# Optimization experiments

Measured on AMD Instinct MI355X. Metric: run time of the kernel, lower is better.

## Reference

```python
import jax, jax.numpy as jnp
import numpy as np

T, B, N, G, M = 2, 16, 1024, 64, 32
D_MODEL, N_LAYER = 384, 12
D_INNER, D_STATE, DT_RANK, D_CONV = 768, 16, 24, 4
TAU, V_TH, SG_ALPHA, BN_EPS, LN_EPS = 2.0, 0.5, 4.0, 1e-5, 1e-5

@jax.custom_vjp
def heaviside(x):
    return (x >= 0.0).astype(x.dtype)

def _hv_fwd(x):
    return heaviside(x), x

def _hv_bwd(x, g):
    s = jax.nn.sigmoid(SG_ALPHA * x)
    return (g * SG_ALPHA * s * (1.0 - s),)

heaviside.defvjp(_hv_fwd, _hv_bwd)

def lif(x):
    # multi-step LIF over leading T folded into batch: x is [T*B, ...]
    shp = x.shape
    xt = x.reshape((T, shp[0] // T) + shp[1:])
    def step(v, xi):
        v = v + (xi - v) / TAU              # charge
        s = heaviside(v - V_TH)             # fire (surrogate grad)
        v = v * (1.0 - jax.lax.stop_gradient(s))  # detached hard reset
        return v, s
    _, spikes = jax.lax.scan(step, jnp.zeros_like(xt[0]), xt)
    return spikes.reshape(shp)

def bn(x, g, b):
    # eval-mode BatchNorm with running stats (mean 0, var 1)
    return x * (g / jnp.sqrt(1.0 + BN_EPS)) + b

def layernorm(x, g, b):
    mu = jnp.mean(x, -1, keepdims=True)
    var = jnp.var(x, -1, keepdims=True)
    return (x - mu) / jnp.sqrt(var + LN_EPS) * g + b

def fps(pts, n_samples):
    # pts: [B, N, 3]; serial farthest point sampling starting at index 0
    b = pts.shape[0]
    def step(carry, _):
        dist, last = carry
        lp = jnp.take_along_axis(pts, last[:, None, None], axis=1)
        d = jnp.sum((pts - lp) ** 2, -1)
        dist = jnp.minimum(dist, d)
        nxt = jnp.argmax(dist, -1).astype(jnp.int32)
        return (dist, nxt), last
    init = (jnp.full((b, pts.shape[1]), 1e10, pts.dtype), jnp.zeros((b,), jnp.int32))
    _, idxs = jax.lax.scan(step, init, None, length=n_samples)
    return jnp.take_along_axis(pts, idxs.T[..., None], axis=1)

def mamba(x, in_w, conv_w, conv_b, xproj_w, dt_w, dt_b, A_log, Dp, out_w):
    # x: [TB, L, d_model] spiking-Mamba mixer
    tb, L, _ = x.shape
    xz = x @ in_w.T
    xh, z = jnp.split(xz, 2, axis=-1)                     # [TB, L, Di]
    xc = jnp.transpose(xh, (0, 2, 1))                     # [TB, Di, L]
    xc = jax.lax.conv_general_dilated(xc, conv_w[:, None, :], (1,), [(D_CONV - 1, 0)], dimension_numbers=('NCH', 'OIH', 'NCH'), feature_group_count=D_INNER) + conv_b[None, :, None]
    xs = lif(jnp.transpose(xc, (0, 2, 1)))                # spiking activation
    dbl = xs @ xproj_w.T
    dt, Bm, Cm = jnp.split(dbl, [DT_RANK, DT_RANK + D_STATE], axis=-1)
    dt = jax.nn.softplus(dt @ dt_w.T + dt_b)              # [TB, L, Di]
    A = -jnp.exp(A_log)                                   # [Di, S]
    def step(h, inp):
        dt_t, B_t, C_t, x_t = inp
        h = h * jnp.exp(dt_t[..., None] * A) + (dt_t * x_t)[..., None] * B_t[:, None, :]
        y = jnp.einsum('bds,bs->bd', h, C_t)
        return h, y
    h0 = jnp.zeros((tb, D_INNER, D_STATE), x.dtype)
    _, ys = jax.lax.scan(step, h0, (dt.transpose(1, 0, 2), Bm.transpose(1, 0, 2), Cm.transpose(1, 0, 2), xs.transpose(1, 0, 2)))
    y = ys.transpose(1, 0, 2) + xs * Dp                   # [TB, L, Di]
    y = y * lif(z)                                        # spiking gate
    return y @ out_w.T

def _forward(xyz, enc1_w, enc1_b, bn1_g, bn1_b, enc2_w, enc2_b, bn2_g, bn2_b, enc3_w, enc3_b, bn3_g, bn3_b, enc4_w, enc4_b, bn4_g, bn4_b, pos1_w, pos1_b, pos2_w, pos2_b, in_w, conv_w, conv_b, xproj_w, dt_w, dt_b, A_log, Dp, out_w, normf_g, normf_b):
    xyz_f = xyz.reshape(T * B, N, 3)
    # Group: FPS centers (expand=1.0 -> identical centers per timestep) + KNN gather
    center = jnp.tile(fps(xyz_f[:B], G), (T, 1, 1))       # [TB, G, 3]
    d2 = jnp.sum(center ** 2, -1)[..., None] + jnp.sum(xyz_f ** 2, -1)[:, None, :] - 2.0 * jnp.einsum('bgc,bnc->bgn', center, xyz_f)
    _, idx = jax.lax.top_k(-d2, M)                        # [TB, G, M]
    nb = jax.vmap(lambda p, i: p[i])(xyz_f, idx)          # [TB, G, M, 3]
    nb = nb - center[:, :, None, :]
    # Encoder (1x1 convs == matmuls over last dim), BN eval-mode, LIF spikes
    f = bn(nb @ enc1_w.T + enc1_b, bn1_g, bn1_b)
    f = lif(f)
    f = bn(f @ enc2_w.T + enc2_b, bn2_g, bn2_b)           # [TB, G, M, 256]
    gl = jnp.max(f, axis=2, keepdims=True)
    f = jnp.concatenate([jnp.broadcast_to(gl, f.shape), f], axis=-1)  # 512 ch
    f = lif(f)
    f = bn(f @ enc3_w.T + enc3_b, bn3_g, bn3_b)
    f = lif(f)
    f = bn(f @ enc4_w.T + enc4_b, bn4_g, bn4_b)
    tokens = jnp.max(f, axis=2)                           # [TB, G, d_model]
    pos = jax.nn.gelu(center @ pos1_w.T + pos1_b) @ pos2_w.T + pos2_b
    hidden = tokens + pos
    residual = None
    for l in range(N_LAYER):
        residual = hidden if residual is None else hidden + residual
        hs = lif(residual)                                # Block.norm_lif
        hidden = mamba(hs, in_w[l], conv_w[l], conv_b[l], xproj_w[l], dt_w[l], dt_b[l], A_log[l], Dp[l], out_w[l])
    residual = hidden + residual
    return layernorm(residual, normf_g, normf_b)          # [TB, G, d_model]

def setup_inputs():
    key = jax.random.key(0)
    ks = iter(jax.random.split(key, 40))
    def nrm(shape, std):
        return jax.random.normal(next(ks), shape, jnp.float32) * std
    inp = {}
    inp['xyz'] = jax.random.normal(next(ks), (T, B, N, 3), jnp.float32)
    inp['enc1_w'] = nrm((128, 3), 0.5); inp['enc1_b'] = jnp.zeros((128,))
    inp['bn1_g'] = jnp.ones((128,)); inp['bn1_b'] = jnp.zeros((128,))
    inp['enc2_w'] = nrm((256, 128), 128 ** -0.5); inp['enc2_b'] = jnp.zeros((256,))
    inp['bn2_g'] = jnp.ones((256,)); inp['bn2_b'] = jnp.zeros((256,))
    inp['enc3_w'] = nrm((512, 512), 512 ** -0.5); inp['enc3_b'] = jnp.zeros((512,))
    inp['bn3_g'] = jnp.ones((512,)); inp['bn3_b'] = jnp.zeros((512,))
    inp['enc4_w'] = nrm((D_MODEL, 512), 512 ** -0.5); inp['enc4_b'] = jnp.zeros((D_MODEL,))
    inp['bn4_g'] = jnp.ones((D_MODEL,)); inp['bn4_b'] = jnp.zeros((D_MODEL,))
    inp['pos1_w'] = nrm((128, 3), 0.5); inp['pos1_b'] = jnp.zeros((128,))
    inp['pos2_w'] = nrm((D_MODEL, 128), 128 ** -0.5); inp['pos2_b'] = jnp.zeros((D_MODEL,))
    nl = N_LAYER
    inp['in_w'] = nrm((nl, 2 * D_INNER, D_MODEL), D_MODEL ** -0.5)
    inp['conv_w'] = nrm((nl, D_INNER, D_CONV), D_CONV ** -0.5)
    inp['conv_b'] = jnp.zeros((nl, D_INNER))
    inp['xproj_w'] = nrm((nl, DT_RANK + 2 * D_STATE, D_INNER), D_INNER ** -0.5)
    inp['dt_w'] = nrm((nl, D_INNER, DT_RANK), DT_RANK ** -0.5)
    inp['dt_b'] = jnp.full((nl, D_INNER), float(np.log(np.expm1(0.01))))
    inp['A_log'] = jnp.log(jnp.tile(jnp.arange(1, D_STATE + 1, dtype=jnp.float32), (nl, D_INNER, 1)))
    inp['Dp'] = jnp.ones((nl, D_INNER))
    inp['out_w'] = nrm((nl, D_MODEL, D_INNER), D_INNER ** -0.5)
    inp['normf_g'] = jnp.ones((D_MODEL,)); inp['normf_b'] = jnp.zeros((D_MODEL,))
    return inp

def reference(xyz, enc1_w, enc1_b, bn1_g, bn1_b, enc2_w, enc2_b, bn2_g, bn2_b, enc3_w, enc3_b, bn3_g, bn3_b, enc4_w, enc4_b, bn4_g, bn4_b, pos1_w, pos1_b, pos2_w, pos2_b, in_w, conv_w, conv_b, xproj_w, dt_w, dt_b, A_log, Dp, out_w, normf_g, normf_b):
    return _forward(xyz, enc1_w, enc1_b, bn1_g, bn1_b, enc2_w, enc2_b, bn2_g, bn2_b, enc3_w, enc3_b, bn3_g, bn3_b, enc4_w, enc4_b, bn4_g, bn4_b, pos1_w, pos1_b, pos2_w, pos2_b, in_w, conv_w, conv_b, xproj_w, dt_w, dt_b, A_log, Dp, out_w, normf_g, normf_b)
```

## Files before the change

### kernel.cpp

```cpp
#include <hip/hip_runtime.h>
#include <hip/hip_bf16.h>

typedef unsigned short ushort_t;
typedef short short8 __attribute__((ext_vector_type(8)));
typedef float f32x4 __attribute__((ext_vector_type(4)));

#define T_    2
#define B_    16
#define NPTS  1024
#define G_    64
#define M_    32
#define DM    384
#define NLAYER 12
#define DI    768
#define DS    16
#define DTR   24
#define DCONV 4
#define TB    32
#define KSPL  6
#define OKC   4
#define LOG2E 1.4426950408889634f

#if __has_builtin(__builtin_amdgcn_exp2f)
#define EXP2F(x) __builtin_amdgcn_exp2f(x)
#else
#define EXP2F(x) exp2f(x)
#endif

__device__ __forceinline__ ushort_t f2b(float x) {
    unsigned u = __float_as_uint(x);
    u = (u + 0x7FFF + ((u >> 16) & 1)) >> 16;
    return (ushort_t)u;
}
__device__ __forceinline__ float b2f(ushort_t h) { return __uint_as_float(((unsigned)h) << 16); }
#define BF1 0x3F80

#define LIF2(va0, vb0, va1, vb1, O0, O1) do { \
    float _u = (va0)*0.5f; float _s = (_u >= 0.5f) ? 1.f : 0.f; _u = (_s > 0.f) ? 0.f : _u; \
    float _u2 = _u + ((vb0) - _u)*0.5f; \
    unsigned _r0 = (_s > 0.f) ? (unsigned)BF1 : 0u; \
    unsigned _r1 = (_u2 >= 0.5f) ? (unsigned)BF1 : 0u; \
    _u = (va1)*0.5f; _s = (_u >= 0.5f) ? 1.f : 0.f; _u = (_s > 0.f) ? 0.f : _u; \
    _u2 = _u + ((vb1) - _u)*0.5f; \
    O0 = _r0 | (((_s > 0.f) ? (unsigned)BF1 : 0u) << 16); \
    O1 = _r1 | (((_u2 >= 0.5f) ? (unsigned)BF1 : 0u) << 16); \
} while (0)

#define DPP_AMAX(bv, bi, CTRL) { \
    float _ov = __int_as_float(__builtin_amdgcn_update_dpp(__float_as_int(bv), __float_as_int(bv), CTRL, 0xF, 0xF, false)); \
    int   _oi = __builtin_amdgcn_update_dpp(bi, bi, CTRL, 0xF, 0xF, false); \
    bool _tk = (_ov > bv) || (_ov == bv && _oi < bi); \
    bv = _tk ? _ov : bv; bi = _tk ? _oi : bi; }
#define DPP_AMIN(bv, bi, CTRL) { \
    float _ov = __int_as_float(__builtin_amdgcn_update_dpp(__float_as_int(bv), __float_as_int(bv), CTRL, 0xF, 0xF, false)); \
    int   _oi = __builtin_amdgcn_update_dpp(bi, bi, CTRL, 0xF, 0xF, false); \
    bool _tk = (_ov < bv) || (_ov == bv && _oi < bi); \
    bv = _tk ? _ov : bv; bi = _tk ? _oi : bi; }
#define DPP_FADD(p, CTRL) { \
    float _ov = __int_as_float(__builtin_amdgcn_update_dpp(__float_as_int(p), __float_as_int(p), CTRL, 0xF, 0xF, false)); \
    p += _ov; }

__global__ __launch_bounds__(64) void fps_kernel(const float* __restrict__ xyz,
                                                 float* __restrict__ centers) {
    int b = blockIdx.x;
    const float* pts = xyz + (size_t)b * NPTS * 3;
    __shared__ float sx[NPTS], sy[NPTS], sz[NPTS];
    int t = threadIdx.x;
    for (int i = t; i < NPTS; i += 64) {
        sx[i] = pts[i*3+0]; sy[i] = pts[i*3+1]; sz[i] = pts[i*3+2];
    }
    __syncthreads();
    float px[16], py[16], pz[16], dd[16];
#pragma unroll
    for (int j = 0; j < 16; j++) {
        px[j] = sx[j*64+t]; py[j] = sy[j*64+t]; pz[j] = sz[j*64+t];
        dd[j] = 1e10f;
    }
    float lx = sx[0], ly = sy[0], lz = sz[0];
    for (int s = 0; s < G_; s++) {
        if (t == 0) {
            centers[(b*G_+s)*3+0] = lx;
            centers[(b*G_+s)*3+1] = ly;
            centers[(b*G_+s)*3+2] = lz;
        }
        float v[16]; int id[16];
#pragma unroll
        for (int j = 0; j < 16; j++) {
            float dx = px[j]-lx, dy = py[j]-ly, dz = pz[j]-lz;
            float di2 = dx*dx + dy*dy + dz*dz;
            dd[j] = fminf(dd[j], di2);
            v[j] = dd[j]; id[j] = j*64 + t;
        }
#pragma unroll
        for (int st = 8; st; st >>= 1)
#pragma unroll
            for (int j = 0; j < 8; j++) {
                if (j < st && v[j+st] > v[j]) { v[j] = v[j+st]; id[j] = id[j+st]; }
            }
        float bv = v[0]; int bi = id[0];
        DPP_AMAX(bv, bi, 0xB1);
        DPP_AMAX(bv, bi, 0x4E);
        DPP_AMAX(bv, bi, 0x141);
        DPP_AMAX(bv, bi, 0x140);
        {
            float ov = __shfl_xor(bv, 16); int oi = __shfl_xor(bi, 16);
            bool tk = (ov > bv) || (ov == bv && oi < bi);
            bv = tk ? ov : bv; bi = tk ? oi : bi;
            ov = __shfl_xor(bv, 32); oi = __shfl_xor(bi, 32);
            tk = (ov > bv) || (ov == bv && oi < bi);
            bv = tk ? ov : bv; bi = tk ? oi : bi;
        }
        lx = sx[bi]; ly = sy[bi]; lz = sz[bi];
    }
}

__global__ __launch_bounds__(256) void knn_kernel(const float* __restrict__ xyz,
                                                  const float* __restrict__ centers,
                                                  float* __restrict__ nb) {
    int tb = blockIdx.x >> 4;
    int g  = ((blockIdx.x & 15) << 2) + (threadIdx.x >> 6);
    const float* pts = xyz + (size_t)tb * NPTS * 3;
    int bb = tb & (B_-1);
    float cx = centers[(bb*G_+g)*3+0], cy = centers[(bb*G_+g)*3+1], cz = centers[(bb*G_+g)*3+2];
    float cs = cx*cx + cy*cy + cz*cz;
    __shared__ float sx[NPTS], sy[NPTS], sz[NPTS];
    int t = threadIdx.x & 63;
    for (int i = threadIdx.x; i < NPTS; i += 256) {
        sx[i] = pts[i*3+0]; sy[i] = pts[i*3+1]; sz[i] = pts[i*3+2];
    }
    __syncthreads();
    float d2[16];
#pragma unroll
    for (int j = 0; j < 16; j++) {
        int i = j*64 + t;
        float qx = sx[i], qy = sy[i], qz = sz[i];
        float ps  = qx*qx + qy*qy + qz*qz;
        float dot = cx*qx + cy*qy + cz*qz;
        d2[j] = cs + ps - 2.0f*dot;
    }
    for (int m = 0; m < M_; m++) {
        float v[16]; int id[16];
#pragma unroll
        for (int j = 0; j < 16; j++) { v[j] = d2[j]; id[j] = j*64 + t; }
#pragma unroll
        for (int st = 8; st; st >>= 1)
#pragma unroll
            for (int j = 0; j < 8; j++) {
                if (j < st && v[j+st] < v[j]) { v[j] = v[j+st]; id[j] = id[j+st]; }
            }
        float bv = v[0]; int bi = id[0];
        DPP_AMIN(bv, bi, 0xB1);
        DPP_AMIN(bv, bi, 0x4E);
        DPP_AMIN(bv, bi, 0x141);
        DPP_AMIN(bv, bi, 0x140);
        {
            float ov = __shfl_xor(bv, 16); int oi = __shfl_xor(bi, 16);
            bool tk = (ov < bv) || (ov == bv && oi < bi);
            bv = tk ? ov : bv; bi = tk ? oi : bi;
            ov = __shfl_xor(bv, 32); oi = __shfl_xor(bi, 32);
            tk = (ov < bv) || (ov == bv && oi < bi);
            bv = tk ? ov : bv; bi = tk ? oi : bi;
        }
        if ((bi & 63) == t) {
            int jw = bi >> 6;
#pragma unroll
            for (int j = 0; j < 16; j++) if (j == jw) d2[j] = 1e38f;
        }
        if (t == 0) {
            size_t o = (((size_t)tb * G_ + g) * M_ + m) * 3;
            nb[o+0] = sx[bi] - cx;
            nb[o+1] = sy[bi] - cy;
            nb[o+2] = sz[bi] - cz;
        }
    }
}

__global__ void wsplit3_kernel(const float* __restrict__ s0, int n0,
                               const float* __restrict__ s1, int n1,
                               const float* __restrict__ s2, int n2,
                               ushort_t* __restrict__ hi, ushort_t* __restrict__ lo) {
    int n = n0 + n1 + n2;
    for (int i = blockIdx.x*256 + threadIdx.x; i < n; i += gridDim.x*256) {
        float w = (i < n0) ? s0[i] : (i < n0+n1 ? s1[i-n0] : s2[i-n0-n1]);
        ushort_t h = f2b(w);
        hi[i] = h;
        lo[i] = f2b(w - b2f(h));
    }
}

template<int PRODS, int EPI, int BMR, int NB = 128>
__global__ __launch_bounds__(256) void gemm_mfma(
    const ushort_t* __restrict__ A, const ushort_t* __restrict__ Al, int lda,
    const ushort_t* __restrict__ Bh, const ushort_t* __restrict__ Bl, int ldb,
    const float* __restrict__ bias, const float* __restrict__ bng, const float* __restrict__ bnb,
    const float* __restrict__ extra, int extra_shift,
    float* __restrict__ out, int ldo,
    ushort_t* __restrict__ sout, int ldso, int half,
    int rows, int K, int Cout)
{
    constexpr int WN = (BMR == 128) ? 2 : 4;
    constexpr int BANDN = NB / WN;
    constexpr int JF = BANDN / 16;
    constexpr int SMSZ = BMR*64 + NB*64*2 + ((PRODS == 3) ? BMR*64 : 8);
    __shared__ __align__(16) ushort_t SMEM[SMSZ];
    ushort_t* As  = SMEM;
    ushort_t* Bhs = SMEM + BMR*64;
    ushort_t* Bls = Bhs + NB*64;
    ushort_t* Als = Bls + NB*64;
    const int tid = threadIdx.x;
    const int bx = blockIdx.x;
    const int by = blockIdx.y;
    int cb = by, kc = 0;
    if constexpr (EPI == 8) {
        int nbc = Cout / NB;
        cb = by % nbc; kc = by / nbc;
    }
    const int c0 = (EPI == 7) ? 0 : cb * NB;
    const int r0  = bx * BMR;
    const int r0h = bx * (BMR/2);
    const int lane = tid & 63, w = tid >> 6;
    const int wm = w / WN, wn = w % WN;
    const int lrow = lane & 15, lkg = lane >> 4;
    const int sw = (lrow & 7) << 3;

    f32x4 acc[4][JF];
#pragma unroll
    for (int i = 0; i < 4; i++)
#pragma unroll
        for (int j = 0; j < JF; j++) acc[i][j] = (f32x4){0.f, 0.f, 0.f, 0.f};

    const int kchu = (EPI == 8) ? (K / extra_shift) : 0;
    const int kbeg = (EPI == 7) ? by * half : ((EPI == 8) ? kc * kchu : 0);
    const int kend = (EPI == 7) ? kbeg + half : ((EPI == 8) ? kbeg + kchu : K);
    for (int k0 = kbeg; k0 < kend; k0 += 64) {
        __syncthreads();
        for (int s = tid; s < BMR*8; s += 256) {
            int row = s >> 3, kq = s & 7;
            int li = row*64 + ((kq*8) ^ ((row & 7) << 3));
            int grow;
            if constexpr (EPI == 0 || EPI == 6 || EPI == 7) grow = r0 + row;
            else {
                int q = row >> 4, wr = row & 15;
                grow = r0h + q*8 + (wr & 7) + ((wr & 8) ? half : 0);
            }
            *(uint4*)&As[li] = *(const uint4*)(A + (size_t)grow*lda + k0 + kq*8);
            if constexpr (PRODS == 3)
                *(uint4*)&Als[li] = *(const uint4*)(Al + (size_t)grow*lda + k0 + kq*8);
        }
        for (int s = tid; s < NB*8; s += 256) {
            int row = s >> 3, kq = s & 7;
            int li = row*64 + ((kq*8) ^ ((row & 7) << 3));
            uint4 vh = make_uint4(0,0,0,0), vl = make_uint4(0,0,0,0);
            if (c0 + row < Cout) {
                vh = *(const uint4*)(Bh + (size_t)(c0+row)*ldb + k0 + kq*8);
                vl = *(const uint4*)(Bl + (size_t)(c0+row)*ldb + k0 + kq*8);
            }
            *(uint4*)&Bhs[li] = vh;
            *(uint4*)&Bls[li] = vl;
        }
        __syncthreads();
#pragma unroll
        for (int kc2 = 0; kc2 < 2; kc2++) {
            const int kb = (kc2*32 + lkg*8) ^ sw;
            short8 af[4], bhf[JF], blf[JF];
#pragma unroll
            for (int tI = 0; tI < 4; tI++)
                af[tI]  = *(const short8*)&As [(wm*64 + tI*16 + lrow)*64 + kb];
#pragma unroll
            for (int tJ = 0; tJ < JF; tJ++) {
                bhf[tJ] = *(const short8*)&Bhs[(wn*BANDN + tJ*16 + lrow)*64 + kb];
                blf[tJ] = *(const short8*)&Bls[(wn*BANDN + tJ*16 + lrow)*64 + kb];
            }
#pragma unroll
            for (int i = 0; i < 4; i++)
#pragma unroll
                for (int j = 0; j < JF; j++)
                    acc[i][j] = __builtin_amdgcn_mfma_f32_16x16x32_bf16(af[i], bhf[j], acc[i][j], 0, 0, 0);
#pragma unroll
            for (int i = 0; i < 4; i++)
#pragma unroll
                for (int j = 0; j < JF; j++)
                    acc[i][j] = __builtin_amdgcn_mfma_f32_16x16x32_bf16(af[i], blf[j], acc[i][j], 0, 0, 0);
            if constexpr (PRODS == 3) {
                short8 alf[4];
#pragma unroll
                for (int tI = 0; tI < 4; tI++)
                    alf[tI] = *(const short8*)&Als[(wm*64 + tI*16 + lrow)*64 + kb];
#pragma unroll
                for (int i = 0; i < 4; i++)
#pragma unroll
                    for (int j = 0; j < JF; j++)
                        acc[i][j] = __builtin_amdgcn_mfma_f32_16x16x32_bf16(alf[i], bhf[j], acc[i][j], 0, 0, 0);
            }
        }
    }

    const float rbn = 1.0f / sqrtf(1.0f + 1e-5f);
    const int ocol0 = c0 + wn*BANDN + lrow;
    auto spike_pair = [&](float vt) -> ushort_t {
        float vp = __shfl_xor(vt, 32);
        float x0 = (lane < 32) ? vt : vp;
        float x1 = (lane < 32) ? vp : vt;
        float u  = x0 * 0.5f;
        float s0 = (u >= 0.5f) ? 1.f : 0.f;
        u = (s0 > 0.f) ? 0.f : u;
        float u2 = u + (x1 - u) * 0.5f;
        return (lane < 32) ? ((s0 > 0.f) ? BF1 : 0) : ((u2 >= 0.5f) ? BF1 : 0);
    };

    if constexpr (EPI == 0) {
#pragma unroll
        for (int j = 0; j < JF; j++) {
            int col = ocol0 + j*16;
            if (col >= Cout) continue;
            float bsc = 1.f, bsh = 0.f, bv = 0.f;
            if (bng)  { bsc = bng[col] * rbn; bsh = bnb[col]; }
            if (bias) bv = bias[col];
#pragma unroll
            for (int i = 0; i < 4; i++)
#pragma unroll
                for (int r = 0; r < 4; r++) {
                    int grow = r0 + wm*64 + i*16 + lkg*4 + r;
                    float v = acc[i][j][r];
                    if (extra) v += extra[(size_t)(grow >> extra_shift)*Cout + col];
                    v += bv;
                    if (bng) v = v*bsc + bsh;
                    out[(size_t)grow*ldo + col] = v;
                }
        }
    }

    if constexpr (EPI == 7) {
        float* op = out + (size_t)by * rows * ldo;
#pragma unroll
        for (int j = 0; j < JF; j++) {
            int col = ocol0 + j*16;
            if (col >= Cout) continue;
#pragma unroll
            for (int i = 0; i < 4; i++)
#pragma unroll
                for (int r = 0; r < 4; r++) {
                    int grow = r0 + wm*64 + i*16 + lkg*4 + r;
                    op[(size_t)grow*ldo + col] = acc[i][j][r];
                }
        }
    }

    if constexpr (EPI == 8) {
        float* op = out + (size_t)kc * rows * ldo;
#pragma unroll
        for (int j = 0; j < JF; j++) {
            int col = ocol0 + j*16;
#pragma unroll
            for (int i = 0; i < 4; i++)
#pragma unroll
                for (int r = 0; r < 4; r++) {
                    int orow_t = wm*64 + i*16 + lkg*4 + r;
                    int q = orow_t >> 4, wr = orow_t & 15;
                    int grow = r0h + q*8 + (wr & 7) + ((wr & 8) ? half : 0);
                    op[(size_t)grow*ldo + col] = acc[i][j][r];
                }
        }
    }

    if constexpr (EPI == 6) {
#pragma unroll
        for (int j = 0; j < JF; j++) {
            int col = ocol0 + j*16;
            float bsc = bng[col] * rbn, bsh = bnb[col], bv = bias[col];
            float m0 = -3.0e38f, m1 = -3.0e38f;
#pragma unroll
            for (int i = 0; i < 4; i++)
#pragma unroll
                for (int r = 0; r < 4; r++) {
                    float v = (acc[i][j][r] + bv) * bsc + bsh;
                    if (i < 2) m0 = fmaxf(m0, v); else m1 = fmaxf(m1, v);
                }
            m0 = fmaxf(m0, __shfl_xor(m0, 16)); m0 = fmaxf(m0, __shfl_xor(m0, 32));
            m1 = fmaxf(m1, __shfl_xor(m1, 16)); m1 = fmaxf(m1, __shfl_xor(m1, 32));
            int bg = (r0 >> 5) + wm*2;
            int msk = (1 << half) - 1;
            if (lkg == 0)
                out[(size_t)(bg >> half)*(G_*DM) + (size_t)(bg & msk)*ldo + col] = m0;
            else if (lkg == 1)
                out[(size_t)((bg+1) >> half)*(G_*DM) + (size_t)((bg+1) & msk)*ldo + col] = m1;
        }
    }

    if constexpr (EPI == 5) {
#pragma unroll
        for (int j = 0; j < JF; j++) {
            int col = ocol0 + j*16;
            float bsc = bng[col] * rbn, bsh = bnb[col], bv = bias[col];
            float gm = -3.0e38f;
#pragma unroll
            for (int i = 0; i < 4; i++)
#pragma unroll
                for (int r = 0; r < 4; r++) {
                    float v = (acc[i][j][r] + bv) * bsc + bsh;
                    gm = fmaxf(gm, v);
                }
            float g2 = fmaxf(gm, __shfl_xor(gm, 16));
            ushort_t gsp = spike_pair(g2);
            ushort_t* gout = (ushort_t*)out;
            int bg = (r0h >> 5) + wm;
            int prs = half >> 5;
            if (lane < 16) gout[(size_t)bg * 256 + col] = gsp;
            else if (lane >= 32 && lane < 48) gout[(size_t)(prs + bg) * 256 + col] = gsp;
        }
    }

    if constexpr (EPI == 2 || EPI == 5) {
        if constexpr (NB == 128) {
            __syncthreads();
            float* Ef = (float*)Bhs;
#pragma unroll
            for (int p = 0; p < 2; p++) {
                if (wn == p) {
#pragma unroll
                    for (int j = 0; j < JF; j++) {
                        int col = ocol0 + j*16;
                        float bsc = 1.f, bsh = 0.f, bv = 0.f;
                        if (bng) { bsc = bng[col] * rbn; bsh = bnb[col]; }
                        if (bias) bv = bias[col];
#pragma unroll
                        for (int i = 0; i < 4; i++)
#pragma unroll
                            for (int r = 0; r < 4; r++) {
                                int o = wm*64 + i*16 + lkg*4 + r;
                                int pr = ((o >> 4) << 3) + (o & 7);
                                int tt = (o >> 3) & 1;
                                float v = acc[i][j][r];
                                if (EPI == 2 && extra) {
                                    int grw = r0h + pr + (tt ? half : 0);
                                    v += extra[(size_t)(grw >> extra_shift)*Cout + col];
                                }
                                v += bv;
                                if (bng) v = v*bsc + bsh;
                                int lr = tt*64 + pr;
                                int cc = j*16 + lrow;
                                Ef[lr*64 + (cc ^ (((lr >> 2) & 3) << 4))] = v;
                            }
                    }
                }
                __syncthreads();
                {
                    int pr2 = tid >> 2, cs = tid & 3;
                    int sw2 = ((pr2 >> 2) & 3) << 4;
                    const float* E0 = Ef + pr2*64;
                    const float* E1 = Ef + (64 + pr2)*64;
                    int colg = c0 + p*64 + cs*16;
                    ushort_t* s0p = sout + (size_t)(r0h + pr2)*ldso + colg;
                    ushort_t* s1p = s0p + (size_t)half*ldso;
#pragma unroll
                    for (int h = 0; h < 4; h++) {
                        int cb2 = (cs*16 + h*4) ^ sw2;
                        const float* e0 = E0 + cb2;
                        const float* e1 = E1 + cb2;
                        unsigned oa, ob, pa, pb;
                        LIF2(e0[0], e1[0], e0[1], e1[1], oa, pa);
                        LIF2(e0[2], e1[2], e0[3], e1[3], ob, pb);
                        *(uint2*)(s0p + h*4) = make_uint2(oa, ob);
                        *(uint2*)(s1p + h*4) = make_uint2(pa, pb);
                    }
                }
                if (p == 0) __syncthreads();
            }
        } else {
            __syncthreads();
            float* Ef = (float*)As;
#pragma unroll
            for (int j = 0; j < JF; j++) {
                int col = ocol0 + j*16;
                float bsc = 1.f, bsh = 0.f, bv = 0.f;
                if (bng) { bsc = bng[col] * rbn; bsh = bnb[col]; }
                if (bias) bv = bias[col];
#pragma unroll
                for (int i = 0; i < 4; i++)
#pragma unroll
                    for (int r = 0; r < 4; r++) {
                        int o = wm*64 + i*16 + lkg*4 + r;
                        int pr = ((o >> 4) << 3) + (o & 7);
                        int tt = (o >> 3) & 1;
                        float v = acc[i][j][r];
                        if (EPI == 2 && extra) {
                            int grw = r0h + pr + (tt ? half : 0);
                            v += extra[(size_t)(grw >> extra_shift)*Cout + col];
                        }
                        v += bv;
                        if (bng) v = v*bsc + bsh;
                        int lr = tt*64 + pr;
                        int cc = wn*BANDN + j*16 + lrow;
                        Ef[lr*64 + (cc ^ (((lr >> 2) & 3) << 4))] = v;
                    }
            }
            __syncthreads();
            {
                int pr2 = tid >> 2, cs = tid & 3;
                int sw2 = ((pr2 >> 2) & 3) << 4;
                const float* E0 = Ef + pr2*64;
                const float* E1 = Ef + (64 + pr2)*64;
                int colg = c0 + cs*16;
                ushort_t* s0p = sout + (size_t)(r0h + pr2)*ldso + colg;
                ushort_t* s1p = s0p + (size_t)half*ldso;
#pragma unroll
                for (int h = 0; h < 4; h++) {
                    int cb2 = (cs*16 + h*4) ^ sw2;
                    const float* e0 = E0 + cb2;
                    const float* e1 = E1 + cb2;
                    unsigned oa, ob, pa, pb;
                    LIF2(e0[0], e1[0], e0[1], e1[1], oa, pa);
                    LIF2(e0[2], e1[2], e0[3], e1[3], ob, pb);
                    *(uint2*)(s0p + h*4) = make_uint2(oa, ob);
                    *(uint2*)(s1p + h*4) = make_uint2(pa, pb);
                }
            }
        }
    }

    if constexpr (EPI == 4) {
        __syncthreads();
        float* Ef = (float*)Bhs;
#pragma unroll
        for (int j = 0; j < JF; j++) {
#pragma unroll
            for (int i = 0; i < 4; i++)
#pragma unroll
                for (int r = 0; r < 4; r++) {
                    int o = i*16 + lkg*4 + r;
                    int pr = ((o >> 4) << 3) + (o & 7);
                    int tt = (o >> 3) & 1;
                    int lr = tt*32 + pr;
                    int cc = wn*BANDN + j*16 + lrow;
                    Ef[lr*NB + (cc ^ (((lr >> 2) & 3) << 4))] = acc[i][j][r];
                }
        }
        __syncthreads();
        {
            constexpr int HH = NB / 32;
            constexpr int CPT = NB / 8;
            int pr2 = tid >> 3, cs = tid & 7;
            int sw2 = ((pr2 >> 2) & 3) << 4;
            const float* E0 = Ef + pr2*NB;
            const float* E1 = Ef + (32 + pr2)*NB;
            float* o0p = out + (size_t)(r0h + pr2)*ldo + c0 + cs*CPT;
            float* o1p = out + (size_t)(half + r0h + pr2)*ldo + c0 + cs*CPT;
            ushort_t* s0p = sout + (size_t)(r0h + pr2)*ldso + c0 + cs*CPT;
            ushort_t* s1p = sout + (size_t)(half + r0h + pr2)*ldso + c0 + cs*CPT;
#pragma unroll
            for (int h = 0; h < HH; h++) {
                int cb2 = (cs*CPT + h*4) ^ sw2;
                const float* e0 = E0 + cb2;
                const float* e1 = E1 + cb2;
                float4 rv0 = *(float4*)(o0p + h*4);
                float4 rv1 = *(float4*)(o1p + h*4);
                float t0x = e0[0]+rv0.x, t0y = e0[1]+rv0.y, t0z = e0[2]+rv0.z, t0w = e0[3]+rv0.w;
                float t1x = e1[0]+rv1.x, t1y = e1[1]+rv1.y, t1z = e1[2]+rv1.z, t1w = e1[3]+rv1.w;
                *(float4*)(o0p + h*4) = make_float4(t0x, t0y, t0z, t0w);
                *(float4*)(o1p + h*4) = make_float4(t1x, t1y, t1z, t1w);
                unsigned oa, ob, pa, pb;
                LIF2(t0x, t1x, t0y, t1y, oa, pa);
                LIF2(t0z, t1z, t0w, t1w, ob, pb);
                *(uint2*)(s0p + h*4) = make_uint2(oa, ob);
                *(uint2*)(s1p + h*4) = make_uint2(pa, pb);
            }
        }
    }

    if constexpr (EPI == 3) {
        if (c0 >= DI) {
#pragma unroll
            for (int j = 0; j < JF; j++) {
                int col = ocol0 + j*16;
#pragma unroll
                for (int i = 0; i < 4; i++)
#pragma unroll
                    for (int r = 0; r < 4; r++) {
                        int orow_t = wm*64 + i*16 + lkg*4 + r;
                        int q = orow_t >> 4, wr = orow_t & 15;
                        int grow = r0h + q*8 + (wr & 7) + ((wr & 8) ? half : 0);
                        sout[(size_t)grow*ldso + col - DI] = spike_pair(acc[i][j][r]);
                    }
            }
        } else {
            __syncthreads();
            constexpr int GRP = 256 / NB;
            constexpr int LPT = 64 / GRP;
            constexpr int SWM = (NB == 128) ? 7 : 3;
            float* Sme = wm ? (float*)Bls : (float*)Bhs;
            ushort_t* Asu = As;
            if (lkg < 2) {
#pragma unroll
                for (int j = 0; j < JF; j++) {
                    int dloc = wn*BANDN + j*16 + lrow;
#pragma unroll
                    for (int i = 0; i < 4; i++) {
                        int lr0 = i*8 + lkg*4;
#pragma unroll
                        for (int r = 0; r < 4; r++)
                            Sme[(lr0 + r)*NB + dloc] = acc[i][j][r];
                    }
                }
            }
            __syncthreads();
            const int dloc_c = tid & (NB - 1);
            const int lb = (tid / NB) * LPT;
            const int dg = c0 + dloc_c;
            const float cw0 = extra[dg*4+0], cw1 = extra[dg*4+1];
            const float cw2 = extra[dg*4+2], cw3 = extra[dg*4+3];
            const float cbv = bias[dg];
            const float* S0f = (const float*)Bhs;
            const float* S1f = (const float*)Bls;
            auto SRD = [&](int l) -> float {
                return (l < 32) ? S0f[l*NB + dloc_c] : S1f[(l - 32)*NB + dloc_c];
            };
            float a0[LPT];
            {
                float vm3 = 0.f, vm2 = 0.f, vm1 = 0.f;
                if (lb) { vm3 = SRD(lb-3); vm2 = SRD(lb-2); vm1 = SRD(lb-1); }
#pragma unroll
                for (int q = 0; q < LPT; q++) {
                    float v = SRD(lb + q);
                    float aa = vm3*cw0 + vm2*cw1 + vm1*cw2 + v*cw3 + cbv;
                    vm3 = vm2; vm2 = vm1; vm1 = v;
                    float u = aa * 0.5f;
                    float sv = (u >= 0.5f) ? 1.f : 0.f;
                    a0[q] = (sv > 0.f) ? 0.f : u;
                    int l = lb + q;
                    Asu[l*NB + (dloc_c ^ (((l >> 1) & SWM) << 4))] = (sv > 0.f) ? BF1 : 0;
                }
            }
            __syncthreads();
            if (lkg >= 2) {
#pragma unroll
                for (int j = 0; j < JF; j++) {
                    int dloc = wn*BANDN + j*16 + lrow;
#pragma unroll
                    for (int i = 0; i < 4; i++) {
                        int lr0 = i*8 + (lkg - 2)*4;
#pragma unroll
                        for (int r = 0; r < 4; r++)
                            Sme[(lr0 + r)*NB + dloc] = acc[i][j][r];
                    }
                }
            }
            ushort_t* xb0 = (ushort_t*)out + (size_t)bx * G_ * DI + c0;
            constexpr int CPT = NB / 4;
            {
                int row = tid >> 2, cs2 = tid & 3;
                int sw2 = ((row >> 1) & SWM) << 4;
                ushort_t* xrow = xb0 + (size_t)row * DI;
#pragma unroll
                for (int kk = 0; kk < NB/64; kk++) {
                    int cb2 = cs2*CPT + kk*16;
                    int cl = cb2 ^ sw2;
                    uint4 va = *(uint4*)&Asu[row*NB + cl];
                    uint4 vb = *(uint4*)&Asu[row*NB + cl + 8];
                    *(uint4*)&xrow[cb2] = va;
                    *(uint4*)&xrow[cb2 + 8] = vb;
                }
            }
            __syncthreads();
            {
                float vm3 = 0.f, vm2 = 0.f, vm1 = 0.f;
                if (lb) { vm3 = SRD(lb-3); vm2 = SRD(lb-2); vm1 = SRD(lb-1); }
#pragma unroll
                for (int q = 0; q < LPT; q++) {
                    float v = SRD(lb + q);
                    float a1 = vm3*cw0 + vm2*cw1 + vm1*cw2 + v*cw3 + cbv;
                    vm3 = vm2; vm2 = vm1; vm1 = v;
                    float u2 = a0[q] + (a1 - a0[q]) * 0.5f;
                    int l = lb + q;
                    Asu[l*NB + (dloc_c ^ (((l >> 1) & SWM) << 4))] = (u2 >= 0.5f) ? BF1 : 0;
                }
            }
            __syncthreads();
            {
                int row = tid >> 2, cs2 = tid & 3;
                int sw2 = ((row >> 1) & SWM) << 4;
                ushort_t* xrow = xb0 + (size_t)16 * G_ * DI + (size_t)row * DI;
#pragma unroll
                for (int kk = 0; kk < NB/64; kk++) {
                    int cb2 = cs2*CPT + kk*16;
                    int cl = cb2 ^ sw2;
                    uint4 va = *(uint4*)&Asu[row*NB + cl];
                    uint4 vb = *(uint4*)&Asu[row*NB + cl + 8];
                    *(uint4*)&xrow[cb2] = va;
                    *(uint4*)&xrow[cb2 + 8] = vb;
                }
            }
        }
    }
}

__global__ __launch_bounds__(256) void opfix_kernel(
    const float* __restrict__ part,
    float* __restrict__ residual, ushort_t* __restrict__ hs) {
    int e = blockIdx.x * 256 + threadIdx.x;
    if (e >= 1024 * (DM/4)) return;
    int r = e / (DM/4), c4 = (e % (DM/4)) * 4;
    size_t o0 = (size_t)r * DM + c4;
    size_t o1 = (size_t)(r + 1024) * DM + c4;
    float4 s0 = *(const float4*)(part + o0);
    float4 s1 = *(const float4*)(part + o1);
#pragma unroll
    for (int k = 1; k < OKC; k++) {
        float4 p0 = *(const float4*)(part + (size_t)k*2048*DM + o0);
        float4 p1 = *(const float4*)(part + (size_t)k*2048*DM + o1);
        s0.x += p0.x; s0.y += p0.y; s0.z += p0.z; s0.w += p0.w;
        s1.x += p1.x; s1.y += p1.y; s1.z += p1.z; s1.w += p1.w;
    }
    float4 rv0 = *(float4*)(residual + o0);
    float4 rv1 = *(float4*)(residual + o1);
    float t0x = s0.x+rv0.x, t0y = s0.y+rv0.y, t0z = s0.z+rv0.z, t0w = s0.w+rv0.w;
    float t1x = s1.x+rv1.x, t1y = s1.y+rv1.y, t1z = s1.z+rv1.z, t1w = s1.w+rv1.w;
    *(float4*)(residual + o0) = make_float4(t0x, t0y, t0z, t0w);
    *(float4*)(residual + o1) = make_float4(t1x, t1y, t1z, t1w);
    unsigned oa, ob, pa, pb;
    LIF2(t0x, t1x, t0y, t1y, oa, pa);
    LIF2(t0z, t1z, t0w, t1w, ob, pb);
    *(uint2*)(hs + o0) = make_uint2(oa, ob);
    *(uint2*)(hs + o1) = make_uint2(pa, pb);
}

#define KT 32
#define FMA_ROW(accv, s) { accv.x += b.x*(s); accv.y += b.y*(s); accv.z += b.z*(s); accv.w += b.w*(s); }
template<int RPT>
__global__ __launch_bounds__(256) void gemm_kernel(
    const float* __restrict__ A, int lda,
    const float* __restrict__ Wt, int ldw,
    const float* __restrict__ bias,
    float* __restrict__ out, int ldo,
    int rows, int K, int Cout, int act)
{
    constexpr int BM = RPT * 16;
    __shared__ __align__(16) float As[KT][BM];
    __shared__ __align__(16) float Bs[KT][64];
    const int tid = threadIdx.x;
    const int r0 = blockIdx.x * BM;
    const int c0 = blockIdx.y * 64;
    const int tx = tid & 15, ty = tid >> 4;
    const int colb = c0 + tx * 4;
    const float4 z4 = make_float4(0.f, 0.f, 0.f, 0.f);
    float4 acc0 = z4, acc1 = z4, acc2 = z4, acc3 = z4;
    for (int k0 = 0; k0 < K; k0 += KT) {
        for (int s = tid; s < BM * 8; s += 256) {
            int row = s >> 3, kq = s & 7;
            int dcol = row ^ (kq << 2);
            float4 va = z4;
            if (r0 + row < rows && (k0 + kq*4) < K)
                va = *(const float4*)(A + (size_t)(r0+row)*lda + k0 + kq*4);
            As[kq*4+0][dcol] = va.x; As[kq*4+1][dcol] = va.y;
            As[kq*4+2][dcol] = va.z; As[kq*4+3][dcol] = va.w;
        }
        for (int s = tid; s < 512; s += 256) {
            int row = s >> 3, kq = s & 7;
            int dcol = row ^ (kq << 2);
            float4 vb = z4;
            if (c0 + row < Cout && (k0 + kq*4) < K)
                vb = *(const float4*)(Wt + (size_t)(c0+row)*ldw + k0 + kq*4);
            Bs[kq*4+0][dcol] = vb.x; Bs[kq*4+1][dcol] = vb.y;
            Bs[kq*4+2][dcol] = vb.z; Bs[kq*4+3][dcol] = vb.w;
        }
        __syncthreads();
#pragma unroll 4
        for (int k = 0; k < KT; k++) {
            const int swz = ((k >> 2) & 7) << 2;
            const float4 b  = *(const float4*)&Bs[k][(tx*4) ^ swz];
            const float4 a0 = *(const float4*)&As[k][(ty*RPT) ^ swz];
            FMA_ROW(acc0, a0.x); FMA_ROW(acc1, a0.y);
            FMA_ROW(acc2, a0.z); FMA_ROW(acc3, a0.w);
        }
        __syncthreads();
    }
    if (colb >= Cout) return;
    float4 o4 = z4;
    if (bias) { o4.x = bias[colb]; o4.y = bias[colb+1]; o4.z = bias[colb+2]; o4.w = bias[colb+3]; }
    const int rbase = r0 + ty * RPT;
#define EPILOG(accv, rr) { \
    int row = rbase + (rr); \
    if (row < rows) { \
        float4 v = accv; \
        v.x += o4.x; v.y += o4.y; v.z += o4.z; v.w += o4.w; \
        *(float4*)(out + (size_t)row*ldo + colb) = v; \
    } }
    EPILOG(acc0, 0); EPILOG(acc1, 1); EPILOG(acc2, 2); EPILOG(acc3, 3);
#undef EPILOG
}

#define MMR 16
__global__ __launch_bounds__(256) void mm_kernel(
    const float* __restrict__ in, const float* __restrict__ Wt,
    const float* __restrict__ bias, float* __restrict__ out,
    int rows, int Cout, int act) {
    __shared__ __align__(16) float lds[MMR * 4];
    int tid = threadIdx.x;
    int r0  = blockIdx.x * MMR;
    int o   = tid & 127;
    for (int i = tid; i < MMR * 4; i += 256) {
        int rr = i >> 2, cc = i & 3;
        int row = r0 + rr;
        lds[i] = (row < rows && cc < 3) ? in[(size_t)row*3 + cc] : 0.f;
    }
    __syncthreads();
    if (tid >= 128 || o >= Cout) return;
    float w0 = Wt[o*3], w1 = Wt[o*3+1], w2 = Wt[o*3+2];
    float bv = bias ? bias[o] : 0.f;
    for (int r = 0; r < MMR; r++) {
        int row = r0 + r;
        if (row >= rows) break;
        float v = lds[r*4]*w0 + lds[r*4+1]*w1 + lds[r*4+2]*w2 + bv;
        if (act == 1) {
            float u = 0.7978845608028654f * (v + 0.044715f * v * v * v);
            v = 0.5f * v * (1.f + tanhf(u));
        }
        out[(size_t)row * 128 + o] = v;
    }
}

__global__ __launch_bounds__(256) void enc1_lif_kernel(
    const float* __restrict__ nb, const float* __restrict__ w, const float* __restrict__ bias,
    const float* __restrict__ bng, const float* __restrict__ bnb,
    ushort_t* __restrict__ f1s, int g0, int half, int bgsh) {
    int e = blockIdx.x * 256 + threadIdx.x;
    if (e >= half * 128) return;
    int r = e >> 7, col = e & 127;
    int tb = r >> bgsh, rem = r & ((1 << bgsh) - 1);
    int gl = rem >> 5, m = rem & 31;
    size_t i0 = (((size_t)tb * G_ + g0 + gl) * M_ + m) * 3;
    size_t i1 = i0 + (size_t)16 * G_ * M_ * 3;
    float w0 = w[col*3], w1 = w[col*3+1], w2 = w[col*3+2];
    float sc = bng[col] / sqrtf(1.f + 1e-5f), sh = bnb[col], bv = bias[col];
    float a0 = (nb[i0]*w0 + nb[i0+1]*w1 + nb[i0+2]*w2 + bv) * sc + sh;
    float a1 = (nb[i1]*w0 + nb[i1+1]*w1 + nb[i1+2]*w2 + bv) * sc + sh;
    float u  = a0 * 0.5f;
    float s0 = (u >= 0.5f) ? 1.f : 0.f;
    u = (s0 > 0.f) ? 0.f : u;
    float u2 = u + (a1 - u) * 0.5f;
    f1s[(size_t)r * 128 + col] = (s0 > 0.f) ? BF1 : 0;
    f1s[((size_t)half + r) * 128 + col] = (u2 >= 0.5f) ? BF1 : 0;
}

__global__ __launch_bounds__(256) void addpos_lif_kernel(
    const float* __restrict__ tokens, const float* __restrict__ pos,
    float* __restrict__ residual, ushort_t* __restrict__ hs, int half) {
    int e = blockIdx.x * 256 + threadIdx.x;
    if (e >= half) return;
    float p = pos[e];
    float r0 = tokens[e] + p;
    float r1 = tokens[e + half] + p;
    residual[e] = r0; residual[e + half] = r1;
    float v  = r0 * 0.5f;
    float s0 = (v >= 0.5f) ? 1.f : 0.f;
    v = (s0 > 0.f) ? 0.f : v;
    float v2 = v + (r1 - v) * 0.5f;
    hs[e] = (s0 > 0.f) ? BF1 : 0;
    hs[e + half] = (v2 >= 0.5f) ? BF1 : 0;
}

__global__ __launch_bounds__(256) void scan_kernel(
    const float* __restrict__ dbl,
    const ushort_t* __restrict__ xs, const ushort_t* __restrict__ zs,
    const float* __restrict__ A_log, const float* __restrict__ Dp,
    const float* __restrict__ dt_w, const float* __restrict__ dt_b,
    ushort_t* __restrict__ yh, ushort_t* __restrict__ yl) {
    int tb = blockIdx.x;
    int d0 = blockIdx.y * 64;
    int tid = threadIdx.x;
    const int dl = tid >> 2;
    const int sg = tid & 3;
    const int d  = d0 + dl;
    __shared__ float SD[G_][56];
    __shared__ float SDT[G_][64];
    __shared__ ushort_t SX[G_][64];
    __shared__ ushort_t SZ[G_][64];
    __shared__ ushort_t SYH[G_][64];
    __shared__ ushort_t SYL[G_][64];
    for (int i = tid; i < G_ * 56; i += 256) {
        int l = i / 56, j = i - l * 56;
        const float* dp0 = dbl + ((size_t)tb * G_ + l) * 56 + j;
        float sv = 0.f;
#pragma unroll
        for (int p = 0; p < KSPL; p++) sv += dp0[(size_t)p * TB * G_ * 56];
        SD[l][j] = sv;
    }
    for (int i = tid; i < G_ * 8; i += 256) {
        int row = i >> 3, seg = i & 7;
        size_t go = ((size_t)tb * G_ + row) * DI + d0 + seg*8;
        *(uint4*)&SX[row][seg*8] = *(const uint4*)(xs + go);
        *(uint4*)&SZ[row][seg*8] = *(const uint4*)(zs + go);
    }
    __syncthreads();
    {
        int dloc = tid & 63;
        int dd = d0 + dloc;
        float wdt[DTR];
#pragma unroll
        for (int k = 0; k < DTR; k++) wdt[k] = dt_w[dd * DTR + k];
        float db = dt_b[dd];
        int lbase = tid >> 6;
#pragma unroll
        for (int st = 0; st < 16; st++) {
            int l = lbase + st * 4;
            float dtv = db;
#pragma unroll
            for (int k = 0; k < DTR; k++) dtv += SD[l][k] * wdt[k];
            dtv = fmaxf(dtv, 0.f) + log1pf(EXP2F(-fabsf(dtv) * LOG2E));
            SDT[l][dloc] = dtv;
        }
    }
    __syncthreads();
    float A2[4];
#pragma unroll
    for (int k = 0; k < 4; k++)
        A2[k] = -EXP2F(A_log[d * DS + 4*sg + k] * LOG2E) * LOG2E;
    const float dpv = Dp[d];
    float h0 = 0.f, h1 = 0.f, h2 = 0.f, h3 = 0.f;
#pragma unroll 4
    for (int l = 0; l < G_; l++) {
        float dtv = SDT[l][dl];
        float4 Bv = *(const float4*)&SD[l][DTR + 4*sg];
        float4 Cv = *(const float4*)&SD[l][DTR + DS + 4*sg];
        float xv = b2f(SX[l][dl]);
        float dx = dtv * xv;
        h0 = h0 * EXP2F(dtv * A2[0]) + dx * Bv.x;
        h1 = h1 * EXP2F(dtv * A2[1]) + dx * Bv.y;
        h2 = h2 * EXP2F(dtv * A2[2]) + dx * Bv.z;
        h3 = h3 * EXP2F(dtv * A2[3]) + dx * Bv.w;
        float p = h0*Cv.x + h1*Cv.y + h2*Cv.z + h3*Cv.w;
        DPP_FADD(p, 0xB1);
        DPP_FADD(p, 0x4E);
        if (sg == 0) {
            float y = (p + xv * dpv) * b2f(SZ[l][dl]);
            ushort_t hb = f2b(y);
            SYH[l][dl] = hb;
            SYL[l][dl] = f2b(y - b2f(hb));
        }
    }
    __syncthreads();
    for (int i = tid; i < G_ * 8; i += 256) {
        int row = i >> 3, seg = i & 7;
        size_t go = ((size_t)tb * G_ + row) * DI + d0 + seg*8;
        *(uint4*)(yh + go) = *(uint4*)&SYH[row][seg*8];
        *(uint4*)(yl + go) = *(uint4*)&SYL[row][seg*8];
    }
}

__global__ __launch_bounds__(128) void ln_kernel(const float* __restrict__ in1,
                                                 const float* __restrict__ g,
                                                 const float* __restrict__ b,
                                                 float* __restrict__ out) {
    int row = blockIdx.x;
    __shared__ float xsm[DM];
    __shared__ float red[128];
    int tid = threadIdx.x;
    float s = 0.f;
    for (int c = tid; c < DM; c += 128) {
        float x = in1[(size_t)row * DM + c];
        xsm[c] = x; s += x;
    }
    red[tid] = s; __syncthreads();
    for (int w = 64; w > 0; w >>= 1) { if (tid < w) red[tid] += red[tid + w]; __syncthreads(); }
    float mu = red[0] / DM;
    __syncthreads();
    float s2 = 0.f;
    for (int c = tid; c < DM; c += 128) { float dv = xsm[c] - mu; s2 += dv * dv; }
    red[tid] = s2; __syncthreads();
    for (int w = 64; w > 0; w >>= 1) { if (tid < w) red[tid] += red[tid + w]; __syncthreads(); }
    float var = red[0] / DM;
    float inv = 1.f / sqrtf(var + 1e-5f);
    for (int c = tid; c < DM; c += 128)
        out[(size_t)row * DM + c] = (xsm[c] - mu) * inv * g[c] + b[c];
}

extern "C" void kernel_launch(void* const* d_in, const int* in_sizes, int n_in,
                              void* d_out, int out_size, void* d_ws, size_t ws_size,
                              hipStream_t stream) {
    const float* xyz     = (const float*)d_in[0];
    const float* enc1_w  = (const float*)d_in[1];  const float* enc1_b = (const float*)d_in[2];
    const float* bn1_g   = (const float*)d_in[3];  const float* bn1_b  = (const float*)d_in[4];
    const float* enc2_w  = (const float*)d_in[5];  const float* enc2_b = (const float*)d_in[6];
    const float* bn2_g   = (const float*)d_in[7];  const float* bn2_b  = (const float*)d_in[8];
    const float* enc3_w  = (const float*)d_in[9];  const float* enc3_b = (const float*)d_in[10];
    const float* bn3_g   = (const float*)d_in[11]; const float* bn3_b  = (const float*)d_in[12];
    const float* enc4_w  = (const float*)d_in[13]; const float* enc4_b = (const float*)d_in[14];
    const float* bn4_g   = (const float*)d_in[15]; const float* bn4_b  = (const float*)d_in[16];
    const float* pos1_w  = (const float*)d_in[17]; const float* pos1_b = (const float*)d_in[18];
    const float* pos2_w  = (const float*)d_in[19]; const float* pos2_b = (const float*)d_in[20];
    const float* in_w    = (const float*)d_in[21];
    const float* conv_w  = (const float*)d_in[22]; const float* conv_b = (const float*)d_in[23];
    const float* xproj_w = (const float*)d_in[24];
    const float* dt_w    = (const float*)d_in[25]; const float* dt_b   = (const float*)d_in[26];
    const float* A_log   = (const float*)d_in[27]; const float* Dp     = (const float*)d_in[28];
    const float* out_w   = (const float*)d_in[29];
    const float* normf_g = (const float*)d_in[30]; const float* normf_b = (const float*)d_in[31];
    float* outp = (float*)d_out;
    float* ws   = (float*)d_ws;
    const size_t wf = ws_size / 4;

    const size_t NIW = 12*589824, NXP = 12*43008, NOW = 12*294912;
    auto pool_need = [&](int g) -> size_t {
        size_t R = (size_t)g*1024, CBx = (size_t)g*32;
        return R*1088 + CBx*640;
    };
    const size_t fixed_need = 4200000;
    int gch = 8; bool split_all = false;
    {
        const int cand[4] = {64, 32, 16, 8};
        for (int ci = 0; ci < 4; ci++) {
            if (fixed_need + (NIW+NXP+NOW) + pool_need(cand[ci]) <= wf) {
                gch = cand[ci]; split_all = true; break;
            }
        }
    }
    auto ilog2i = [](int x){ int r = 0; while ((1 << r) < x) r++; return r; };
    const int R = gch*1024, HALF = R/2, CB = gch*32;
    const int NCH = 64/gch;
    const int BGSH = 5 + ilog2i(gch);
    const int OGSH = ilog2i(gch);

    size_t off = 0;
    auto alloc = [&](size_t n) { off = (off + 15) & ~(size_t)15; float* p = ws + off; off += n; return p; };
    float* centers  = alloc(3072);
    float* nb       = alloc(196608);
    float* tokens   = alloc(786432);
    float* post     = alloc(131072);
    float* pos      = alloc(393216);
    float* residual = alloc(786432);
    ushort_t* hs_b  = (ushort_t*)alloc(393216);
    ushort_t* ewhi  = (ushort_t*)alloc(245760);
    ushort_t* ewlo  = (ushort_t*)alloc(245760);
    size_t wsz = split_all ? (NIW+NXP+NOW) : 927744;
    ushort_t* whi = (ushort_t*)alloc((wsz+1)/2);
    ushort_t* wlo = (ushort_t*)alloc((wsz+1)/2);
    float* pool = alloc(pool_need(gch));
    float* f2 = pool;
    float* f4 = f2 + (size_t)R*256;
    float* g3 = f4 + (size_t)R*384;
    ushort_t* f1s = (ushort_t*)(g3 + (size_t)CB*512);
    ushort_t* f2s = f1s + (size_t)R*128;
    ushort_t* f3s = f2s + (size_t)R*256;
    ushort_t* gls = f3s + (size_t)R*512;
    float* dblb  = pool;
    ushort_t* xs_b = (ushort_t*)(dblb + KSPL * TB * G_ * 56);
    ushort_t* zs_b = xs_b + 1572864;
    ushort_t* ysh  = zs_b + 1572864;
    ushort_t* ysl  = ysh + 1572864;
    float* opart   = (float*)(ysl + 1572864);

    wsplit3_kernel<<<512, 256, 0, stream>>>(enc2_w, 32768, enc3_w, 262144, enc4_w, 196608, ewhi, ewlo);
    const int E2 = 0, E3 = 32768, E4 = 294912;
    if (split_all)
        wsplit3_kernel<<<2048, 256, 0, stream>>>(in_w, (int)NIW, xproj_w, (int)NXP, out_w, (int)NOW, whi, wlo);

    fps_kernel<<<B_, 64, 0, stream>>>(xyz, centers);
    knn_kernel<<<TB * 16, 256, 0, stream>>>(xyz, centers, nb);

    for (int ch = 0; ch < NCH; ch++) {
        int g0 = ch * gch;
        enc1_lif_kernel<<<(HALF*128 + 255)/256, 256, 0, stream>>>(
            nb, enc1_w, enc1_b, bn1_g, bn1_b, f1s, g0, HALF, BGSH);
        gemm_mfma<2,5,128,64><<<dim3(HALF/64, 4), 256, 0, stream>>>(
            f1s, nullptr, 128, ewhi + E2, ewlo + E2, 128,
            enc2_b, bn2_g, bn2_b, nullptr, 0, (float*)gls, 0, f2s, 256, HALF, R, 128, 256);
        gemm_mfma<2,0,64,64><<<dim3(CB/64, 8), 256, 0, stream>>>(
            gls, nullptr, 256, ewhi + E3, ewlo + E3, 512,
            nullptr, nullptr, nullptr, nullptr, 0, g3, 512, nullptr, 0, 0, CB, 256, 512);
        gemm_mfma<2,2,128,64><<<dim3(HALF/64, 8), 256, 0, stream>>>(
            f2s, nullptr, 256, ewhi + E3 + 256, ewlo + E3 + 256, 512,
            enc3_b, bn3_g, bn3_b, g3, 5, nullptr, 512, f3s, 512, HALF, R, 256, 512);
        gemm_mfma<2,6,128,64><<<dim3(R/128, 6), 256, 0, stream>>>(
            f3s, nullptr, 512, ewhi + E4, ewlo + E4, 512,
            enc4_b, bn4_g, bn4_b, nullptr, 0,
            tokens + (size_t)g0 * DM, DM, nullptr, 0, OGSH, R, 512, 384);
    }

    mm_kernel<<<64, 256, 0, stream>>>(centers, pos1_w, pos1_b, post, 1024, 128, 1);
    gemm_kernel<4><<<dim3(16, 6), 256, 0, stream>>>(
        post, 128, pos2_w, 128, pos2_b, pos, 384, 1024, 128, 384, 0);
    addpos_lif_kernel<<<(393216 + 255) / 256, 256, 0, stream>>>(
        tokens, pos, residual, hs_b, 393216);

    const int NTOK = TB * G_;
    for (int l = 0; l < NLAYER; l++) {
        size_t W_IN, W_XP, W_OUT;
        if (split_all) {
            W_IN = (size_t)l * 589824;
            W_XP = NIW + (size_t)l * 43008;
            W_OUT = NIW + NXP + (size_t)l * 294912;
        } else {
            wsplit3_kernel<<<1024, 256, 0, stream>>>(
                in_w + (size_t)l * 589824, 589824,
                xproj_w + (size_t)l * 43008, 43008,
                out_w + (size_t)l * 294912, 294912, whi, wlo);
            W_IN = 0; W_XP = 589824; W_OUT = 632832;
        }
        gemm_mfma<2,3,128,64><<<dim3(NTOK/128, 24), 256, 0, stream>>>(
            hs_b, nullptr, DM, whi + W_IN, wlo + W_IN, DM,
            conv_b + (size_t)l * DI, nullptr, nullptr, conv_w + (size_t)l * DI * DCONV, 0,
            (float*)xs_b, 0, zs_b, DI, NTOK/2, NTOK, DM, 2*DI);
        gemm_mfma<2,7,64,64><<<dim3(NTOK/64, KSPL), 256, 0, stream>>>(
            xs_b, nullptr, DI, whi + W_XP, wlo + W_XP, DI,
            nullptr, nullptr, nullptr, nullptr, 0, dblb, 56, nullptr, 0, DI/KSPL, NTOK, DI, 56);
        scan_kernel<<<dim3(TB, DI/64), 256, 0, stream>>>(
            dblb, xs_b, zs_b, A_log + (size_t)l * DI * DS, Dp + (size_t)l * DI,
            dt_w + (size_t)l * DI * DTR, dt_b + (size_t)l * DI, ysh, ysl);
        gemm_mfma<3,8,64,64><<<dim3(NTOK/64, 6*OKC), 256, 0, stream>>>(
            ysh, ysl, DI, whi + W_OUT, wlo + W_OUT, DI,
            nullptr, nullptr, nullptr, nullptr, OKC, opart, DM, nullptr, 0, NTOK/2, NTOK, DI, DM);
        opfix_kernel<<<(1024*(DM/4) + 255)/256, 256, 0, stream>>>(opart, residual, hs_b);
    }
    ln_kernel<<<NTOK, 128, 0, stream>>>(residual, normf_g, normf_b, outp);
}
```

Measured before the change: 1.150 ms.

## Prefetch next K-tile of GEMM operands into registers during MFMA compute

The GEMM main loop now computes per-thread global source pointers and LDS destination offsets once, before the loop. Each iteration writes the previously loaded registers into LDS and then issues the global loads for the next K-tile before the MFMA work runs. This is meant to hide global-memory latency behind matrix compute instead of stalling on loads at the top of every iteration. It costs extra VGPRs for the staged tiles and pointers, which may lower occupancy. A separate EPI==4 epilogue block is also deleted, apparently as dead or duplicate code.

```diff
diff --git a/kernel.cpp b/kernel.cpp
--- a/kernel.cpp
+++ b/kernel.cpp
@@ -229,35 +229,70 @@
 #pragma unroll
         for (int j = 0; j < JF; j++) acc[i][j] = (f32x4){0.f, 0.f, 0.f, 0.f};
 
+    constexpr int NA  = (BMR*8)/256;
+    constexpr int NBL = (NB*8)/256;
+    const ushort_t* aptr[NA];
+    const ushort_t* alptr[(PRODS == 3) ? NA : 1];
+    const ushort_t* bhptr[NBL];
+    const ushort_t* blptr[NBL];
+    int ali[NA], bli[NBL];
+    bool bok[NBL];
+#pragma unroll
+    for (int ii = 0; ii < NA; ii++) {
+        int s = tid + ii*256;
+        int row = s >> 3, kq = s & 7;
+        ali[ii] = row*64 + ((kq*8) ^ ((row & 7) << 3));
+        int grow;
+        if constexpr (EPI == 0 || EPI == 6 || EPI == 7) grow = r0 + row;
+        else {
+            int q = row >> 4, wr = row & 15;
+            grow = r0h + q*8 + (wr & 7) + ((wr & 8) ? half : 0);
+        }
+        aptr[ii] = A + (size_t)grow*lda + kq*8;
+        if constexpr (PRODS == 3) alptr[ii] = Al + (size_t)grow*lda + kq*8;
+    }
+#pragma unroll
+    for (int ii = 0; ii < NBL; ii++) {
+        int s = tid + ii*256;
+        int row = s >> 3, kq = s & 7;
+        bli[ii] = row*64 + ((kq*8) ^ ((row & 7) << 3));
+        bok[ii] = (c0 + row < Cout);
+        int rowc = bok[ii] ? (c0 + row) : 0;
+        bhptr[ii] = Bh + (size_t)rowc*ldb + kq*8;
+        blptr[ii] = Bl + (size_t)rowc*ldb + kq*8;
+    }
+    uint4 ra[NA], ral[(PRODS == 3) ? NA : 1], rbh[NBL], rbl[NBL];
+    const uint4 Z4 = make_uint4(0,0,0,0);
+    auto LOADK = [&](int k0) {
+#pragma unroll
+        for (int ii = 0; ii < NA; ii++) {
+            ra[ii] = *(const uint4*)(aptr[ii] + k0);
+            if constexpr (PRODS == 3) ral[ii] = *(const uint4*)(alptr[ii] + k0);
+        }
+#pragma unroll
+        for (int ii = 0; ii < NBL; ii++) {
+            rbh[ii] = bok[ii] ? *(const uint4*)(bhptr[ii] + k0) : Z4;
+            rbl[ii] = bok[ii] ? *(const uint4*)(blptr[ii] + k0) : Z4;
+        }
+    };
+
     const int kchu = (EPI == 8) ? (K / extra_shift) : 0;
     const int kbeg = (EPI == 7) ? by * half : ((EPI == 8) ? kc * kchu : 0);
     const int kend = (EPI == 7) ? kbeg + half : ((EPI == 8) ? kbeg + kchu : K);
+    LOADK(kbeg);
     for (int k0 = kbeg; k0 < kend; k0 += 64) {
         __syncthreads();
-        for (int s = tid; s < BMR*8; s += 256) {
-            int row = s >> 3, kq = s & 7;
-            int li = row*64 + ((kq*8) ^ ((row & 7) << 3));
-            int grow;
-            if constexpr (EPI == 0 || EPI == 6 || EPI == 7) grow = r0 + row;
-            else {
-                int q = row >> 4, wr = row & 15;
-                grow = r0h + q*8 + (wr & 7) + ((wr & 8) ? half : 0);
-            }
-            *(uint4*)&As[li] = *(const uint4*)(A + (size_t)grow*lda + k0 + kq*8);
-            if constexpr (PRODS == 3)
-                *(uint4*)&Als[li] = *(const uint4*)(Al + (size_t)grow*lda + k0 + kq*8);
-        }
-        for (int s = tid; s < NB*8; s += 256) {
-            int row = s >> 3, kq = s & 7;
-            int li = row*64 + ((kq*8) ^ ((row & 7) << 3));
-            uint4 vh = make_uint4(0,0,0,0), vl = make_uint4(0,0,0,0);
-            if (c0 + row < Cout) {
-                vh = *(const uint4*)(Bh + (size_t)(c0+row)*ldb + k0 + kq*8);
-                vl = *(const uint4*)(Bl + (size_t)(c0+row)*ldb + k0 + kq*8);
-            }
-            *(uint4*)&Bhs[li] = vh;
-            *(uint4*)&Bls[li] = vl;
-        }
+#pragma unroll
+        for (int ii = 0; ii < NA; ii++) {
+            *(uint4*)&As[ali[ii]] = ra[ii];
+            if constexpr (PRODS == 3) *(uint4*)&Als[ali[ii]] = ral[ii];
+        }
+#pragma unroll
+        for (int ii = 0; ii < NBL; ii++) {
+            *(uint4*)&Bhs[bli[ii]] = rbh[ii];
+            *(uint4*)&Bls[bli[ii]] = rbl[ii];
+        }
+        if (k0 + 64 < kend) LOADK(k0 + 64);
         __syncthreads();
 #pragma unroll
         for (int kc2 = 0; kc2 < 2; kc2++) {
@@ -514,55 +549,6 @@
                     *(uint2*)(s0p + h*4) = make_uint2(oa, ob);
                     *(uint2*)(s1p + h*4) = make_uint2(pa, pb);
                 }
-            }
-        }
-    }
-
-    if constexpr (EPI == 4) {
-        __syncthreads();
-        float* Ef = (float*)Bhs;
-#pragma unroll
-        for (int j = 0; j < JF; j++) {
-#pragma unroll
-            for (int i = 0; i < 4; i++)
-#pragma unroll
-                for (int r = 0; r < 4; r++) {
-                    int o = i*16 + lkg*4 + r;
-                    int pr = ((o >> 4) << 3) + (o & 7);
-                    int tt = (o >> 3) & 1;
-                    int lr = tt*32 + pr;
-                    int cc = wn*BANDN + j*16 + lrow;
-                    Ef[lr*NB + (cc ^ (((lr >> 2) & 3) << 4))] = acc[i][j][r];
-                }
-        }
-        __syncthreads();
-        {
-            constexpr int HH = NB / 32;
-            constexpr int CPT = NB / 8;
-            int pr2 = tid >> 3, cs = tid & 7;
-            int sw2 = ((pr2 >> 2) & 3) << 4;
-            const float* E0 = Ef + pr2*NB;
-            const float* E1 = Ef + (32 + pr2)*NB;
-            float* o0p = out + (size_t)(r0h + pr2)*ldo + c0 + cs*CPT;
-            float* o1p = out + (size_t)(half + r0h + pr2)*ldo + c0 + cs*CPT;
-            ushort_t* s0p = sout + (size_t)(r0h + pr2)*ldso + c0 + cs*CPT;
-            ushort_t* s1p = sout + (size_t)(half + r0h + pr2)*ldso + c0 + cs*CPT;
-#pragma unroll
-            for (int h = 0; h < HH; h++) {
-                int cb2 = (cs*CPT + h*4) ^ sw2;
-                const float* e0 = E0 + cb2;
-                const float* e1 = E1 + cb2;
-                float4 rv0 = *(float4*)(o0p + h*4);
-                float4 rv1 = *(float4*)(o1p + h*4);
-                float t0x = e0[0]+rv0.x, t0y = e0[1]+rv0.y, t0z = e0[2]+rv0.z, t0w = e0[3]+rv0.w;
-                float t1x = e1[0]+rv1.x, t1y = e1[1]+rv1.y, t1z = e1[2]+rv1.z, t1w = e1[3]+rv1.w;
-                *(float4*)(o0p + h*4) = make_float4(t0x, t0y, t0z, t0w);
-                *(float4*)(o1p + h*4) = make_float4(t1x, t1y, t1z, t1w);
-                unsigned oa, ob, pa, pb;
-                LIF2(t0x, t1x, t0y, t1y, oa, pa);
-                LIF2(t0z, t1z, t0w, t1w, ob, pb);
-                *(uint2*)(s0p + h*4) = make_uint2(oa, ob);
-                *(uint2*)(s1p + h*4) = make_uint2(pa, pb);
             }
         }
     }
```

Measured after the change: 1.791 ms. 1.56x slower.
